# Optimization experiments

Hardware: AMD Instinct MI355X
Metric: run time of the kernel (lower is better)

## Reference

```python
import jax, jax.numpy as jnp
import numpy as np

VOCAB, D = 32000, 1024
EPS = 1e-5

def setup_inputs() -> dict:
    key = jax.random.key(0)
    k1, k2, k3, k4 = jax.random.split(key, 4)
    patch_embeddings = jax.random.normal(k1, (16, 256, D), dtype=jnp.float32)
    text_prototypes = jax.random.normal(k2, (VOCAB, D), dtype=jnp.float32) * 0.02
    # nn.Linear(d, d): weight [d, d], bias [d]
    lim = 1.0 / np.sqrt(D)
    W = jax.random.uniform(k3, (D, D), minval=-lim, maxval=lim, dtype=jnp.float32)
    b = jax.random.uniform(k4, (D,), minval=-lim, maxval=lim, dtype=jnp.float32)
    gamma = jnp.ones((D,), dtype=jnp.float32)
    beta = jnp.zeros((D,), dtype=jnp.float32)
    return {"patch_embeddings": patch_embeddings, "text_prototypes": text_prototypes,
            "W": W, "b": b, "gamma": gamma, "beta": beta}

def _layer_norm(x, gamma, beta):
    mu = jnp.mean(x, axis=-1, keepdims=True)
    var = jnp.mean(jnp.square(x - mu), axis=-1, keepdims=True)
    return (x - mu) * jax.lax.rsqrt(var + EPS) * gamma + beta

def reference(patch_embeddings, text_prototypes, W, b, gamma, beta):
    # similarities: [B, P, V]
    sims = jnp.einsum('bpd,vd->bpv', patch_embeddings, text_prototypes)
    attn = jax.nn.softmax(sims, axis=-1)
    reprogrammed = jnp.einsum('bpv,vd->bpd', attn, text_prototypes)
    transformed = jnp.einsum('bpd,ed->bpe', reprogrammed, W) + b
    return _layer_norm(patch_embeddings + transformed, gamma, beta)
```

## Files before the change

kernel.cpp:

```cpp
#include <hip/hip_runtime.h>
#include <hip/hip_bf16.h>
#include <cstdint>
#include <cstddef>

#define D_DIM 1024
#define VOCAB 32000
#define ROWS  4096

typedef __attribute__((ext_vector_type(8))) short bf16x8;
typedef __attribute__((ext_vector_type(4))) float f32x4;
typedef __attribute__((ext_vector_type(4))) int   i32x4;
typedef __attribute__((ext_vector_type(8))) int   i32x8;

static __device__ __forceinline__ i32x8 cat8(i32x4 lo, i32x4 hi) {
  return __builtin_shufflevector(lo, hi, 0, 1, 2, 3, 4, 5, 6, 7);
}

static __device__ __forceinline__ unsigned short f2bf(float f) {
  union { float f; unsigned int u; } c; c.f = f;
  unsigned int u = c.u;
  u += 0x7fffu + ((u >> 16) & 1u);
  return (unsigned short)(u >> 16);
}

static __device__ __forceinline__ int pk8(float a, float b) {
  return __builtin_amdgcn_cvt_pk_fp8_f32(a, b, 0, false);
}

static __device__ __forceinline__ void gload_lds16(const void* g, void* s) {
  __builtin_amdgcn_global_load_lds(
      (const __attribute__((address_space(1))) uint32_t*)(g),
      (__attribute__((address_space(3))) uint32_t*)(s), 16, 0, 0);
}

__global__ void k_cvt(const float* __restrict__ src, short* __restrict__ dst, int n4) {
  int i = blockIdx.x * 256 + threadIdx.x;
  if (i < n4) {
    float4 v = *(const float4*)(src + (size_t)i * 4);
    ushort4 u;
    u.x = f2bf(v.x); u.y = f2bf(v.y); u.z = f2bf(v.z); u.w = f2bf(v.w);
    *(ushort4*)(dst + (size_t)i * 4) = u;
  }
}

__global__ void k_cvt_q8(const float* __restrict__ src, uint8_t* __restrict__ dst) {
  int i = blockIdx.x * 256 + threadIdx.x;
  float4 a = *(const float4*)(src + (size_t)i * 8);
  float4 b = *(const float4*)(src + (size_t)i * 8 + 4);
  uint2 o;
  o.x = (pk8(a.x, a.y) & 0xffff) | (pk8(a.z, a.w) << 16);
  o.y = (pk8(b.x, b.y) & 0xffff) | (pk8(b.z, b.w) << 16);
  *(uint2*)(dst + (size_t)i * 8) = o;
}

__global__ void k_prep_K8(const float* __restrict__ src, uint8_t* __restrict__ kb,
                          uint8_t* __restrict__ kt, int R, int C) {
  __shared__ uint8_t tile[64][68];
  int t  = threadIdx.x;
  int r0 = blockIdx.x * 64;
  int c0 = blockIdx.y * 64;
  int lr = t >> 4;
  int lc = (t & 15) * 4;
#pragma unroll
  for (int i = 0; i < 4; ++i) {
    int r = lr + 16 * i;
    float4 v = *(const float4*)(src + (size_t)(r0 + r) * C + c0 + lc);
    unsigned p = (pk8(v.x * 64.f, v.y * 64.f) & 0xffff) | (pk8(v.z * 64.f, v.w * 64.f) << 16);
    *(unsigned*)&tile[r][lc] = p;
    *(unsigned*)(kb + (size_t)(r0 + r) * C + c0 + lc) = p;
  }
  __syncthreads();
#pragma unroll
  for (int i = 0; i < 4; ++i) {
    int c = lr + 16 * i;
    unsigned p = tile[lc + 0][c] | (tile[lc + 1][c] << 8) |
                 (tile[lc + 2][c] << 16) | ((unsigned)tile[lc + 3][c] << 24);
    *(unsigned*)(kt + (size_t)(c0 + c) * R + r0 + lc) = p;
  }
}

#define PS1 272
#define G1NT 8
__global__ __launch_bounds__(512)
__attribute__((amdgpu_waves_per_eu(2)))
void k_g1(
    const uint8_t* __restrict__ A,
    const uint8_t* __restrict__ B,
    uint8_t* __restrict__ Pout, float* __restrict__ den)
{
  __shared__ uint8_t smem[131072];

  int tid  = threadIdx.x;
  int wave = tid >> 6;
  int lane = tid & 63;
  int quad = lane >> 4;
  int t16  = lane & 15;
  int wm = wave >> 1;
  int wn = wave & 1;

  int swz = (blockIdx.x & 7) * 250 + (blockIdx.x >> 3);
  int nt  = swz >> 4;
  int mt  = swz & 15;
  long mBase = (long)mt * 256;
  long nBase = (long)nt * 256;

  const uint8_t* Ab = A + (size_t)mBase * D_DIM;
  const uint8_t* Bb = B + (size_t)nBase * D_DIM;
  int lrow = lane >> 3;
  int lcol = ((lane & 7) ^ lrow) * 16;

  f32x4 acc[4][8];
#pragma unroll
  for (int i = 0; i < 4; ++i)
#pragma unroll
    for (int j = 0; j < 8; ++j) acc[i][j] = (f32x4){0.f, 0.f, 0.f, 0.f};

  int sw  = t16 & 7;
  int co0 = (((quad << 1) ^ sw) << 4);
  const int SC1 = 0x7F7F7F7F;

  auto STAGE = [&](int slot, int t) {
    uint8_t* As = &smem[slot * 65536];
    uint8_t* Bs = As + 32768;
    int kk = t * 128;
#pragma unroll
    for (int g = 0; g < 4; ++g) {
      int r0 = wave * 32 + g * 8;
      gload_lds16(Ab + (size_t)(r0 + lrow) * D_DIM + kk + lcol, As + r0 * 128);
    }
#pragma unroll
    for (int g = 0; g < 4; ++g) {
      int r0 = wave * 32 + g * 8;
      gload_lds16(Bb + (size_t)(r0 + lrow) * D_DIM + kk + lcol, Bs + r0 * 128);
    }
  };

  STAGE(0, 0);
  STAGE(1, 1);

  for (int t = 0; t < G1NT; ++t) {
    if (t + 1 < G1NT)
      asm volatile("s_waitcnt vmcnt(8)\n\ts_barrier" ::: "memory");
    else
      asm volatile("s_waitcnt vmcnt(0)\n\ts_barrier" ::: "memory");

    const uint8_t* As = &smem[(t & 1) * 65536];
    const uint8_t* Bs = As + 32768;

    i32x8 am[4];
#pragma unroll
    for (int mi = 0; mi < 4; ++mi) {
      const uint8_t* rp = &As[(wm * 64 + mi * 16 + t16) * 128];
      am[mi] = cat8(*(const i32x4*)(rp + co0), *(const i32x4*)(rp + (co0 ^ 16)));
    }
    __builtin_amdgcn_s_setprio(1);
#pragma unroll
    for (int ni = 0; ni < 8; ++ni) {
      const uint8_t* rp = &Bs[(wn * 128 + ni * 16 + t16) * 128];
      i32x8 bfr = cat8(*(const i32x4*)(rp + co0), *(const i32x4*)(rp + (co0 ^ 16)));
#pragma unroll
      for (int mi = 0; mi < 4; ++mi)
        acc[mi][ni] = __builtin_amdgcn_mfma_scale_f32_16x16x128_f8f6f4(
            am[mi], bfr, acc[mi][ni], 0, 0, 0, SC1, 0, SC1);
    }
    __builtin_amdgcn_s_setprio(0);
    asm volatile("s_barrier" ::: "memory");
    if (t + 2 < G1NT) STAGE(t & 1, t + 2);
  }

  float rsum[4][4];
#pragma unroll
  for (int mi = 0; mi < 4; ++mi)
#pragma unroll
    for (int r = 0; r < 4; ++r) rsum[mi][r] = 0.f;
#pragma unroll
  for (int mi = 0; mi < 4; ++mi) {
    int rloc = wm * 64 + mi * 16 + quad * 4;
#pragma unroll
    for (int ni = 0; ni < 8; ++ni) {
      int cloc = wn * 128 + ni * 16 + t16;
#pragma unroll
      for (int r = 0; r < 4; ++r) {
        float e = __expf(acc[mi][ni][r] * 0.015625f);
        smem[(rloc + r) * PS1 + cloc] = (uint8_t)pk8(e, e);
        rsum[mi][r] += e;
      }
    }
  }
#pragma unroll
  for (int mi = 0; mi < 4; ++mi)
#pragma unroll
    for (int r = 0; r < 4; ++r) {
      float s = rsum[mi][r];
      s += __shfl_xor(s, 1);
      s += __shfl_xor(s, 2);
      s += __shfl_xor(s, 4);
      s += __shfl_xor(s, 8);
      if (t16 == 0)
        atomicAdd(&den[mBase + wm * 64 + mi * 16 + quad * 4 + r], s);
    }
  __syncthreads();
  int rr  = tid >> 4;
  int c16 = (tid & 15) * 16;
#pragma unroll
  for (int i = 0; i < 8; ++i) {
    int row = i * 32 + rr;
    i32x4 v = *(const i32x4*)&smem[row * PS1 + c16];
    __builtin_nontemporal_store(v, (i32x4*)&Pout[(size_t)(mBase + row) * VOCAB + nBase + c16]);
  }
}

__global__ __launch_bounds__(512)
__attribute__((amdgpu_waves_per_eu(2)))
void k_g2(
    const uint8_t* __restrict__ P, const uint8_t* __restrict__ KT,
    float* __restrict__ s0, float* __restrict__ s1, float* __restrict__ s2)
{
  __shared__ uint8_t smem[131072];

  int tid  = threadIdx.x;
  int wave = tid >> 6;
  int lane = tid & 63;
  int quad = lane >> 4;
  int t16  = lane & 15;
  int wm = wave >> 1;
  int wn = wave & 1;

  int bid = blockIdx.x;
  int x   = bid & 7;
  int g   = bid >> 3;
  int dt  = x & 3;
  int zz  = (x >> 2) * 2 + (g >> 4);
  int mt  = g & 15;
  long mBase = (long)mt * 256;
  long dBase = (long)dt * 256;
  int  nsteps = (zz < 2) ? 63 : 62;
  long k0 = ((long)zz * 62 + (zz < 2 ? zz : 2)) * 128;

  const uint8_t* Ab = P  + (size_t)mBase * VOCAB + k0;
  const uint8_t* Bb = KT + (size_t)dBase * VOCAB + k0;
  int lrow = lane >> 3;
  int lcol = ((lane & 7) ^ lrow) * 16;

  f32x4 acc[4][8];
#pragma unroll
  for (int i = 0; i < 4; ++i)
#pragma unroll
    for (int j = 0; j < 8; ++j) acc[i][j] = (f32x4){0.f, 0.f, 0.f, 0.f};

  int sw  = t16 & 7;
  int co0 = (((quad << 1) ^ sw) << 4);
  const int SC1 = 0x7F7F7F7F;

  auto STAGE = [&](int slot, int t) {
    uint8_t* As = &smem[slot * 65536];
    uint8_t* Bs = As + 32768;
    long kk = (long)t * 128;
#pragma unroll
    for (int gi = 0; gi < 4; ++gi) {
      int r0 = wave * 32 + gi * 8;
      gload_lds16(Ab + (size_t)(r0 + lrow) * VOCAB + kk + lcol, As + r0 * 128);
    }
#pragma unroll
    for (int gi = 0; gi < 4; ++gi) {
      int r0 = wave * 32 + gi * 8;
      gload_lds16(Bb + (size_t)(r0 + lrow) * VOCAB + kk + lcol, Bs + r0 * 128);
    }
  };

  STAGE(0, 0);
  STAGE(1, 1);

  for (int t = 0; t < nsteps; ++t) {
    if (t + 1 < nsteps)
      asm volatile("s_waitcnt vmcnt(8)\n\ts_barrier" ::: "memory");
    else
      asm volatile("s_waitcnt vmcnt(0)\n\ts_barrier" ::: "memory");

    const uint8_t* As = &smem[(t & 1) * 65536];
    const uint8_t* Bs = As + 32768;

    i32x8 am[4];
#pragma unroll
    for (int mi = 0; mi < 4; ++mi) {
      const uint8_t* rp = &As[(wm * 64 + mi * 16 + t16) * 128];
      am[mi] = cat8(*(const i32x4*)(rp + co0), *(const i32x4*)(rp + (co0 ^ 16)));
    }
    __builtin_amdgcn_s_setprio(1);
#pragma unroll
    for (int ni = 0; ni < 8; ++ni) {
      const uint8_t* rp = &Bs[(wn * 128 + ni * 16 + t16) * 128];
      i32x8 bfr = cat8(*(const i32x4*)(rp + co0), *(const i32x4*)(rp + (co0 ^ 16)));
#pragma unroll
      for (int mi = 0; mi < 4; ++mi)
        acc[mi][ni] = __builtin_amdgcn_mfma_scale_f32_16x16x128_f8f6f4(
            am[mi], bfr, acc[mi][ni], 0, 0, 0, SC1, 0, SC1);
    }
    __builtin_amdgcn_s_setprio(0);
    asm volatile("s_barrier" ::: "memory");
    if (t + 2 < nsteps) STAGE(t & 1, t + 2);
  }

  float* outp = (zz == 1) ? s1 : (zz == 3) ? s2 : s0;
  bool plain = (zz == 1) || (zz == 3);
#pragma unroll
  for (int mi = 0; mi < 4; ++mi) {
    long row = mBase + wm * 64 + mi * 16 + quad * 4;
#pragma unroll
    for (int ni = 0; ni < 8; ++ni) {
      long col = dBase + wn * 128 + ni * 16 + t16;
#pragma unroll
      for (int r = 0; r < 4; ++r) {
        float* p = &outp[(size_t)(row + r) * D_DIM + col];
        if (plain) *p = acc[mi][ni][r];
        else       atomicAdd(p, acc[mi][ni][r]);
      }
    }
  }
}

__global__ __launch_bounds__(256) void k_gemm_bf(
    const short* __restrict__ A, int lda,
    const short* __restrict__ B, int ldb, int Kdim,
    const float* __restrict__ bias, const float* __restrict__ resid,
    float* __restrict__ Cout)
{
  __shared__ short smem[16384];
  short* As = smem;
  short* Bs = smem + 8192;

  int tid  = threadIdx.x;
  int wave = tid >> 6;
  int lane = tid & 63;
  int quad = lane >> 4;
  int t16  = lane & 15;
  int wy = wave >> 1, wx = wave & 1;

  long mBase = (long)blockIdx.y * 128;
  long nBase = (long)blockIdx.x * 128;

  const short* Ab = A + (size_t)mBase * lda;
  const short* Bb = B + (size_t)nBase * ldb;
  int lrow = lane >> 3;
  int lcol = ((lane & 7) ^ lrow) * 8;

  f32x4 acc[4][4];
#pragma unroll
  for (int i = 0; i < 4; ++i)
#pragma unroll
    for (int j = 0; j < 4; ++j) acc[i][j] = (f32x4){0.f, 0.f, 0.f, 0.f};

  int sw = t16 & 7;

  for (int kk = 0; kk < Kdim; kk += 64) {
#pragma unroll
    for (int i = 0; i < 4; ++i) {
      int row = wave * 32 + i * 8;
      gload_lds16(Ab + (size_t)(row + lrow) * lda + kk + lcol, &As[row * 64]);
      gload_lds16(Bb + (size_t)(row + lrow) * ldb + kk + lcol, &Bs[row * 64]);
    }
    __syncthreads();
#pragma unroll
    for (int kc = 0; kc < 8; kc += 4) {
      bf16x8 af[4], bfr[4];
#pragma unroll
      for (int mi = 0; mi < 4; ++mi)
        af[mi] = *(const bf16x8*)&As[(wy * 64 + mi * 16 + t16) * 64 +
                                     (((kc + quad) ^ sw) << 3)];
#pragma unroll
      for (int ni = 0; ni < 4; ++ni)
        bfr[ni] = *(const bf16x8*)&Bs[(wx * 64 + ni * 16 + t16) * 64 +
                                      (((kc + quad) ^ sw) << 3)];
#pragma unroll
      for (int mi = 0; mi < 4; ++mi)
#pragma unroll
        for (int ni = 0; ni < 4; ++ni)
          acc[mi][ni] = __builtin_amdgcn_mfma_f32_16x16x32_bf16(af[mi], bfr[ni],
                                                                acc[mi][ni], 0, 0, 0);
    }
    __syncthreads();
  }

#pragma unroll
  for (int mi = 0; mi < 4; ++mi) {
    long row = mBase + wy * 64 + mi * 16 + quad * 4;
#pragma unroll
    for (int ni = 0; ni < 4; ++ni) {
      long col = nBase + wx * 64 + ni * 16 + t16;
#pragma unroll
      for (int r = 0; r < 4; ++r) {
        size_t idx = (size_t)(row + r) * 1024 + col;
        Cout[idx] = acc[mi][ni][r] + bias[col] + resid[idx];
      }
    }
  }
}

__global__ void k_div(const float* __restrict__ s0, const float* __restrict__ s1,
                      const float* __restrict__ s2,
                      const float* __restrict__ den, short* __restrict__ out) {
  int i = (blockIdx.x * 256 + threadIdx.x) * 4;
  float4 a = *(const float4*)(s0 + i);
  float4 b = *(const float4*)(s1 + i);
  float4 c = *(const float4*)(s2 + i);
  float inv = 0.015625f / den[i >> 10];
  ushort4 u;
  u.x = f2bf((a.x + b.x + c.x) * inv); u.y = f2bf((a.y + b.y + c.y) * inv);
  u.z = f2bf((a.z + b.z + c.z) * inv); u.w = f2bf((a.w + b.w + c.w) * inv);
  *(ushort4*)(out + i) = u;
}

__global__ __launch_bounds__(256) void k_ln(const float* __restrict__ x,
                                            const float* __restrict__ gamma,
                                            const float* __restrict__ beta,
                                            float* __restrict__ out) {
  __shared__ float s_sum[4], s_sq[4];
  int row = blockIdx.x;
  int tid = threadIdx.x;
  const float* xr = x + (size_t)row * 1024;
  float4 v = *(const float4*)(xr + tid * 4);
  float s = v.x + v.y + v.z + v.w;
  float q = v.x * v.x + v.y * v.y + v.z * v.z + v.w * v.w;
#pragma unroll
  for (int off = 32; off >= 1; off >>= 1) {
    s += __shfl_down(s, off);
    q += __shfl_down(q, off);
  }
  int wv = tid >> 6;
  if ((tid & 63) == 0) { s_sum[wv] = s; s_sq[wv] = q; }
  __syncthreads();
  float tot  = s_sum[0] + s_sum[1] + s_sum[2] + s_sum[3];
  float totq = s_sq[0] + s_sq[1] + s_sq[2] + s_sq[3];
  float mu   = tot * (1.0f / 1024.0f);
  float var  = totq * (1.0f / 1024.0f) - mu * mu;
  float rstd = rsqrtf(var + 1e-5f);
  float4 g = *(const float4*)(gamma + tid * 4);
  float4 b = *(const float4*)(beta + tid * 4);
  float4 o;
  o.x = (v.x - mu) * rstd * g.x + b.x;
  o.y = (v.y - mu) * rstd * g.y + b.y;
  o.z = (v.z - mu) * rstd * g.z + b.z;
  o.w = (v.w - mu) * rstd * g.w + b.w;
  *(float4*)(out + (size_t)row * 1024 + tid * 4) = o;
}

extern "C" void kernel_launch(void* const* d_in, const int* in_sizes, int n_in,
                              void* d_out, int out_size, void* d_ws, size_t ws_size,
                              hipStream_t stream) {
  const float* patch = (const float*)d_in[0];
  const float* proto = (const float*)d_in[1];
  const float* W     = (const float*)d_in[2];
  const float* bvec  = (const float*)d_in[3];
  const float* gamma = (const float*)d_in[4];
  const float* beta  = (const float*)d_in[5];
  float* out = (float*)d_out;

  char* ws = (char*)d_ws;
  size_t off = 0;
  uint8_t* Q8  = (uint8_t*)(ws + off); off += (size_t)ROWS * D_DIM;
  uint8_t* Kb8 = (uint8_t*)(ws + off); off += (size_t)VOCAB * D_DIM;
  uint8_t* KT8 = (uint8_t*)(ws + off); off += (size_t)VOCAB * D_DIM;
  short*   Wb  = (short*)(ws + off);   off += (size_t)D_DIM * D_DIM * 2;
  short*   Rb  = (short*)(ws + off);   off += (size_t)ROWS * D_DIM * 2;
  uint8_t* P8  = (uint8_t*)(ws + off); off += (size_t)ROWS * VOCAB;
  float*   num = (float*)(ws + off);   off += (size_t)ROWS * D_DIM * 4;
  float*   den = (float*)(ws + off);   off += (size_t)ROWS * 4;
  float*   pre = (float*)P8;
  float*   sz0 = (float*)(ws);
  float*   sz1 = (float*)(ws + (size_t)16 * 1024 * 1024);
  float*   sz2 = num;

  hipMemsetAsync(den, 0, ROWS * sizeof(float), stream);

  k_cvt_q8<<<ROWS * D_DIM / 8 / 256, 256, 0, stream>>>(patch, Q8);
  k_cvt<<<D_DIM * D_DIM / 4 / 256, 256, 0, stream>>>(W, Wb, D_DIM * D_DIM / 4);
  k_prep_K8<<<dim3(VOCAB / 64, D_DIM / 64), 256, 0, stream>>>(proto, Kb8, KT8, VOCAB, D_DIM);

  k_g1<<<2000, 512, 0, stream>>>(Q8, Kb8, P8, den);

  hipMemsetAsync(sz0, 0, (size_t)16 * 1024 * 1024, stream);

  k_g2<<<256, 512, 0, stream>>>(P8, KT8, sz0, sz1, sz2);

  k_div<<<ROWS * D_DIM / 4 / 256, 256, 0, stream>>>(sz0, sz1, sz2, den, Rb);

  k_gemm_bf<<<dim3(D_DIM / 128, ROWS / 128), 256, 0, stream>>>(
      Rb, D_DIM, Wb, D_DIM, D_DIM, bvec, patch, pre);

  k_ln<<<ROWS, 256, 0, stream>>>(pre, gamma, beta, out);
}
```

Before: 632.6 us.

## Merge prep kernels into one launch and fold normalization into final GEMM prologue

The memset of den, the patch fp8 conversion, the W bf16 conversion and the prototype fp8 transpose-prep are merged into a single k_prep launch dispatched by block index. The separate k_div kernel is removed. Its three-way partial-sum reduction, divide by den and bf16 conversion now run as a prologue inside k_gemm_bf, which writes Rb and then synchronizes before the MFMA loop. Every column block with the same mBase redundantly recomputes and rewrites the same 128 rows of Rb. That multiplies reads of the fp32 partial sums by the number of column blocks, in exchange for fewer launches.

```diff
diff --git a/kernel.cpp b/kernel.cpp
--- a/kernel.cpp
+++ b/kernel.cpp
@@ -33,41 +33,50 @@
       (__attribute__((address_space(3))) uint32_t*)(s), 16, 0, 0);
 }
 
-__global__ void k_cvt(const float* __restrict__ src, short* __restrict__ dst, int n4) {
-  int i = blockIdx.x * 256 + threadIdx.x;
-  if (i < n4) {
-    float4 v = *(const float4*)(src + (size_t)i * 4);
+__global__ __launch_bounds__(256) void k_prep(
+    const float* __restrict__ patch, const float* __restrict__ proto,
+    const float* __restrict__ W,
+    uint8_t* __restrict__ Q8, uint8_t* __restrict__ kb, uint8_t* __restrict__ kt,
+    short* __restrict__ Wb, float* __restrict__ den)
+{
+  __shared__ uint8_t tile[64][68];
+  int bid = blockIdx.x;
+  int t   = threadIdx.x;
+
+  if (bid < 16) {
+    den[bid * 256 + t] = 0.f;
+    return;
+  }
+  if (bid < 2064) {
+    int i = (bid - 16) * 256 + t;
+    float4 a = *(const float4*)(patch + (size_t)i * 8);
+    float4 b = *(const float4*)(patch + (size_t)i * 8 + 4);
+    uint2 o;
+    o.x = (pk8(a.x, a.y) & 0xffff) | (pk8(a.z, a.w) << 16);
+    o.y = (pk8(b.x, b.y) & 0xffff) | (pk8(b.z, b.w) << 16);
+    *(uint2*)(Q8 + (size_t)i * 8) = o;
+    return;
+  }
+  if (bid < 3088) {
+    int i = (bid - 2064) * 256 + t;
+    float4 v = *(const float4*)(W + (size_t)i * 4);
     ushort4 u;
     u.x = f2bf(v.x); u.y = f2bf(v.y); u.z = f2bf(v.z); u.w = f2bf(v.w);
-    *(ushort4*)(dst + (size_t)i * 4) = u;
-  }
-}
-
-__global__ void k_cvt_q8(const float* __restrict__ src, uint8_t* __restrict__ dst) {
-  int i = blockIdx.x * 256 + threadIdx.x;
-  float4 a = *(const float4*)(src + (size_t)i * 8);
-  float4 b = *(const float4*)(src + (size_t)i * 8 + 4);
-  uint2 o;
-  o.x = (pk8(a.x, a.y) & 0xffff) | (pk8(a.z, a.w) << 16);
-  o.y = (pk8(b.x, b.y) & 0xffff) | (pk8(b.z, b.w) << 16);
-  *(uint2*)(dst + (size_t)i * 8) = o;
-}
-
-__global__ void k_prep_K8(const float* __restrict__ src, uint8_t* __restrict__ kb,
-                          uint8_t* __restrict__ kt, int R, int C) {
-  __shared__ uint8_t tile[64][68];
-  int t  = threadIdx.x;
-  int r0 = blockIdx.x * 64;
-  int c0 = blockIdx.y * 64;
+    *(ushort4*)(Wb + (size_t)i * 4) = u;
+    return;
+  }
+  int b  = bid - 3088;
+  int r0 = (b % 500) * 64;
+  int c0 = (b / 500) * 64;
   int lr = t >> 4;
   int lc = (t & 15) * 4;
 #pragma unroll
   for (int i = 0; i < 4; ++i) {
     int r = lr + 16 * i;
-    float4 v = *(const float4*)(src + (size_t)(r0 + r) * C + c0 + lc);
+    float4 v = *(const float4*)(proto + (size_t)(r0 + r) * D_DIM + c0 + lc);
     unsigned p = (pk8(v.x * 64.f, v.y * 64.f) & 0xffff) | (pk8(v.z * 64.f, v.w * 64.f) << 16);
     *(unsigned*)&tile[r][lc] = p;
-    *(unsigned*)(kb + (size_t)(r0 + r) * C + c0 + lc) = p;
+    *(unsigned*)(kb + (size_t)(r0 + r) * D_DIM + c0 + lc) = p;
   }
   __syncthreads();
 #pragma unroll
@@ -75,7 +84,7 @@
     int c = lr + 16 * i;
     unsigned p = tile[lc + 0][c] | (tile[lc + 1][c] << 8) |
                  (tile[lc + 2][c] << 16) | ((unsigned)tile[lc + 3][c] << 24);
-    *(unsigned*)(kt + (size_t)(c0 + c) * R + r0 + lc) = p;
+    *(unsigned*)(kt + (size_t)(c0 + c) * VOCAB + r0 + lc) = p;
   }
 }
 
@@ -320,8 +329,9 @@
 }
 
 __global__ __launch_bounds__(256) void k_gemm_bf(
-    const short* __restrict__ A, int lda,
-    const short* __restrict__ B, int ldb, int Kdim,
+    short* __restrict__ Rb, const short* __restrict__ Bw,
+    const float* __restrict__ s0, const float* __restrict__ s1,
+    const float* __restrict__ s2, const float* __restrict__ den,
     const float* __restrict__ bias, const float* __restrict__ resid,
     float* __restrict__ Cout)
 {
@@ -339,8 +349,24 @@
   long mBase = (long)blockIdx.y * 128;
   long nBase = (long)blockIdx.x * 128;
 
-  const short* Ab = A + (size_t)mBase * lda;
-  const short* Bb = B + (size_t)nBase * ldb;
+#pragma unroll 4
+  for (int j = 0; j < 128; ++j) {
+    size_t e = (size_t)(j * 256 + tid) * 4;
+    size_t gidx = (size_t)mBase * 1024 + e;
+    float4 a = *(const float4*)(s0 + gidx);
+    float4 b = *(const float4*)(s1 + gidx);
+    float4 c = *(const float4*)(s2 + gidx);
+    float inv = 0.015625f / den[gidx >> 10];
+    ushort4 u;
+    u.x = f2bf((a.x + b.x + c.x) * inv); u.y = f2bf((a.y + b.y + c.y) * inv);
+    u.z = f2bf((a.z + b.z + c.z) * inv); u.w = f2bf((a.w + b.w + c.w) * inv);
+    *(ushort4*)(Rb + gidx) = u;
+  }
+  asm volatile("s_waitcnt vmcnt(0)" ::: "memory");
+  __syncthreads();
+
+  const short* Ab = Rb + (size_t)mBase * 1024;
+  const short* Bb = Bw + (size_t)nBase * 1024;
   int lrow = lane >> 3;
   int lcol = ((lane & 7) ^ lrow) * 8;
 
@@ -352,12 +378,12 @@
 
   int sw = t16 & 7;
 
-  for (int kk = 0; kk < Kdim; kk += 64) {
+  for (int kk = 0; kk < 1024; kk += 64) {
 #pragma unroll
     for (int i = 0; i < 4; ++i) {
       int row = wave * 32 + i * 8;
-      gload_lds16(Ab + (size_t)(row + lrow) * lda + kk + lcol, &As[row * 64]);
-      gload_lds16(Bb + (size_t)(row + lrow) * ldb + kk + lcol, &Bs[row * 64]);
+      gload_lds16(Ab + (size_t)(row + lrow) * 1024 + kk + lcol, &As[row * 64]);
+      gload_lds16(Bb + (size_t)(row + lrow) * 1024 + kk + lcol, &Bs[row * 64]);
     }
     __syncthreads();
 #pragma unroll
@@ -394,20 +420,6 @@
       }
     }
   }
-}
-
-__global__ void k_div(const float* __restrict__ s0, const float* __restrict__ s1,
-                      const float* __restrict__ s2,
-                      const float* __restrict__ den, short* __restrict__ out) {
-  int i = (blockIdx.x * 256 + threadIdx.x) * 4;
-  float4 a = *(const float4*)(s0 + i);
-  float4 b = *(const float4*)(s1 + i);
-  float4 c = *(const float4*)(s2 + i);
-  float inv = 0.015625f / den[i >> 10];
-  ushort4 u;
-  u.x = f2bf((a.x + b.x + c.x) * inv); u.y = f2bf((a.y + b.y + c.y) * inv);
-  u.z = f2bf((a.z + b.z + c.z) * inv); u.w = f2bf((a.w + b.w + c.w) * inv);
-  *(ushort4*)(out + i) = u;
 }
 
 __global__ __launch_bounds__(256) void k_ln(const float* __restrict__ x,
@@ -470,11 +482,7 @@
   float*   sz1 = (float*)(ws + (size_t)16 * 1024 * 1024);
   float*   sz2 = num;
 
-  hipMemsetAsync(den, 0, ROWS * sizeof(float), stream);
-
-  k_cvt_q8<<<ROWS * D_DIM / 8 / 256, 256, 0, stream>>>(patch, Q8);
-  k_cvt<<<D_DIM * D_DIM / 4 / 256, 256, 0, stream>>>(W, Wb, D_DIM * D_DIM / 4);
-  k_prep_K8<<<dim3(VOCAB / 64, D_DIM / 64), 256, 0, stream>>>(proto, Kb8, KT8, VOCAB, D_DIM);
+  k_prep<<<11088, 256, 0, stream>>>(patch, proto, W, Q8, Kb8, KT8, Wb, den);
 
   k_g1<<<2000, 512, 0, stream>>>(Q8, Kb8, P8, den);
 
@@ -482,10 +490,8 @@
 
   k_g2<<<256, 512, 0, stream>>>(P8, KT8, sz0, sz1, sz2);
 
-  k_div<<<ROWS * D_DIM / 4 / 256, 256, 0, stream>>>(sz0, sz1, sz2, den, Rb);
-
   k_gemm_bf<<<dim3(D_DIM / 128, ROWS / 128), 256, 0, stream>>>(
-      Rb, D_DIM, Wb, D_DIM, D_DIM, bvec, patch, pre);
+      Rb, Wb, sz0, sz1, sz2, den, bvec, patch, pre);
 
   k_ln<<<ROWS, 256, 0, stream>>>(pre, gamma, beta, out);
 }
```

After: 674.7 us. +6.7%, slower.
